# Kernel tuning notes

Hardware: AMD Instinct MI355X
Metric: run time of the kernel (lower is better)

The kernel has to match this reference:

```python
import jax, jax.numpy as jnp
import numpy as np
from jax import lax

K = 8192
D = 256
BETA = 0.1
DECAY = 0.99
EPS = 1e-05


def setup_inputs() -> dict:
    key = jax.random.key(0)
    k1, k2, k3 = jax.random.split(key, 3)
    z_e = jax.random.normal(k1, (8, 2048, D), dtype=jnp.float32)
    codebook = jax.random.normal(k2, (K, D), dtype=jnp.float32)
    ema_cluster_size = jnp.zeros((K,), dtype=jnp.float32)
    ema_w = jax.random.normal(k3, (K, D), dtype=jnp.float32)
    return {"z_e": z_e, "codebook": codebook,
            "ema_cluster_size": ema_cluster_size, "ema_w": ema_w}


def reference(z_e, codebook, ema_cluster_size, ema_w):
    B, L, Dd = z_e.shape
    # squared-distance matrix (B, L, K): ||z||^2 - 2 z.C^T + ||c||^2
    dist = ((z_e ** 2).sum(-1, keepdims=True)
            - 2.0 * jnp.einsum('bld,kd->blk', z_e, codebook)
            + (codebook ** 2).sum(-1))
    codes = jnp.argmin(dist, axis=-1)          # (B, L) int
    z_q = codebook[codes]                      # gather (B, L, D)

    # training-mode EMA statistics (segment_sum == one_hot.T @ z_e, memory-light)
    flat_codes = codes.reshape(-1)
    flat_z = z_e.reshape(-1, Dd)
    n_i = jax.ops.segment_sum(jnp.ones(flat_codes.shape, dtype=z_e.dtype),
                              flat_codes, num_segments=K)
    dw = jax.ops.segment_sum(flat_z, flat_codes, num_segments=K)
    new_cluster_size = DECAY * ema_cluster_size + (1.0 - DECAY) * n_i
    new_ema_w = DECAY * ema_w + (1.0 - DECAY) * dw
    new_codebook = new_ema_w / (new_cluster_size + EPS)[:, None]

    # straight-through combine and commitment loss
    z_q_st = z_e + lax.stop_gradient(z_q - z_e)
    vq_loss = BETA * jnp.mean((z_e - lax.stop_gradient(z_q)) ** 2)
    return z_q_st, codes, vq_loss, new_codebook, new_cluster_size, new_ema_w
```

## Files before the change

### kernel.cpp

```cpp
#include <hip/hip_runtime.h>
#include <hip/hip_bf16.h>
#include <math.h>

#define N_ROWS 16384
#define DIM    256
#define KCODES 8192

#define OFF_ZQ    0
#define OFF_CODES 4194304
#define OFF_LOSS  4210688
#define OFF_CB    4210689
#define OFF_CS    6307841
#define OFF_EW    6316033
#define OUT_TOTAL 8413185

typedef __attribute__((ext_vector_type(8))) short bf16x8;
typedef __attribute__((ext_vector_type(4))) float f32x4;
typedef __attribute__((ext_vector_type(16))) float f32x16;

__device__ __forceinline__ void gll16(const void* g, void* l) {
  __builtin_amdgcn_global_load_lds(
      (const __attribute__((address_space(1))) unsigned int*)g,
      (__attribute__((address_space(3))) unsigned int*)l, 16, 0, 0);
}

__device__ __forceinline__ unsigned short f2bf(float x) {
  __hip_bfloat16 h = __float2bfloat16(x);
  return *reinterpret_cast<unsigned short*>(&h);
}

__device__ __forceinline__ unsigned umin32(unsigned a, unsigned b) { return a < b ? a : b; }
__device__ __forceinline__ unsigned umax32(unsigned a, unsigned b) { return a > b ? a : b; }

__global__ __launch_bounds__(256) void k_pre(
    const float* __restrict__ z, unsigned short* __restrict__ zbuf,
    const float* __restrict__ cb, unsigned short* __restrict__ cbt,
    float* __restrict__ cnormb, int* __restrict__ cnt,
    float* __restrict__ loss_part) {
  const int b = blockIdx.x;
  const int tid = threadIdx.x;
  if (b < 2048) {
    int i = b * 256 + tid;
    const float4 a = ((const float4*)z)[i * 2];
    const float4 c = ((const float4*)z)[i * 2 + 1];
    union { unsigned short u[8]; uint4 v; } o;
    o.u[0] = f2bf(a.x); o.u[1] = f2bf(a.y); o.u[2] = f2bf(a.z); o.u[3] = f2bf(a.w);
    o.u[4] = f2bf(c.x); o.u[5] = f2bf(c.y); o.u[6] = f2bf(c.z); o.u[7] = f2bf(c.w);
    ((uint4*)zbuf)[i] = o.v;
  } else if (b < 3072) {
    const int code = (b - 2048) * 8 + (tid >> 5);
    const int dq = tid & 31;
    const float4 v0 = *(const float4*)(cb + (size_t)code * 256 + dq * 8);
    const float4 v1 = *(const float4*)(cb + (size_t)code * 256 + dq * 8 + 4);
    union { unsigned short u[8]; uint4 q; } o;
    o.u[0] = f2bf(-2.f * v0.x); o.u[1] = f2bf(-2.f * v0.y);
    o.u[2] = f2bf(-2.f * v0.z); o.u[3] = f2bf(-2.f * v0.w);
    o.u[4] = f2bf(-2.f * v1.x); o.u[5] = f2bf(-2.f * v1.y);
    o.u[6] = f2bf(-2.f * v1.z); o.u[7] = f2bf(-2.f * v1.w);
    *(uint4*)(cbt + ((size_t)dq * 8192 + code) * 8) = o.q;
    float s = v0.x * v0.x + v0.y * v0.y + v0.z * v0.z + v0.w * v0.w +
              v1.x * v1.x + v1.y * v1.y + v1.z * v1.z + v1.w * v1.w;
#pragma unroll
    for (int off = 16; off >= 1; off >>= 1) s += __shfl_down(s, off);
    if ((tid & 31) == 0) cnormb[code] = s + 1024.0f;
  } else if (cnt) {
    int zi = (b - 3072) * 256 + tid;
    if (zi < 8192) cnt[zi] = 0;
    else if (zi < 8448) loss_part[zi - 8192] = 0.0f;
  }
}

__global__ __launch_bounds__(256, 2) void k_argmin(
    const unsigned short* __restrict__ zb,
    const unsigned short* __restrict__ cbt,
    const float* __restrict__ cnb,
    unsigned long long* __restrict__ partials) {
  __shared__ __align__(16) unsigned char lds[69632];

  const int tid = threadIdx.x;
  const int lane = tid & 63;
  const int w = tid >> 6;
  const int wc = w & 1;
  const int wr = w >> 1;
  const int hi = lane >> 5;
  const int l31 = lane & 31;
  const int chunk = blockIdx.x;
  const int r0 = blockIdx.y << 7;

  {
    const char* zgb = (const char*)zb + (size_t)r0 * 512;
#pragma unroll
    for (int it = 0; it < 16; ++it) {
      int s = it * 256 + tid;
      int row = s >> 5;
      int dql = (tid & 31) ^ (row & 31);
      gll16(zgb + row * 512 + dql * 16, lds + s * 16);
    }
    gll16((const char*)cnb + (size_t)chunk * 4096 + tid * 16,
          lds + 65536 + tid * 16);
  }
  asm volatile("s_waitcnt vmcnt(0)" ::: "memory");
  __builtin_amdgcn_s_barrier();
  __builtin_amdgcn_sched_barrier(0);

  bf16x8 zr0[16], zr1[16];
  {
    const int xr = l31 * 16;
    const int rb0 = (wr * 64 + l31) * 512;
    const int rb1 = (wr * 64 + 32 + l31) * 512;
    const int hx = hi * 16;
#pragma unroll
    for (int ks = 0; ks < 16; ++ks) {
      zr0[ks] = *(const bf16x8*)(lds + rb0 + ((ks * 32 + hx) ^ xr));
      zr1[ks] = *(const bf16x8*)(lds + rb1 + ((ks * 32 + hx) ^ xr));
    }
  }
  asm volatile("s_waitcnt lgkmcnt(0)" ::: "memory");
  __builtin_amdgcn_s_barrier();
  __builtin_amdgcn_sched_barrier(0);

  unsigned char* lcb = lds + tid * 16;
  const char* cgc = (const char*)cbt +
      ((size_t)(tid >> 7) * 131072 + (size_t)chunk * 16384 + (tid & 127) * 16);
  gll16(cgc + 0 * 262144, lcb + 0 * 4096);
  gll16(cgc + 1 * 262144, lcb + 1 * 4096);
  gll16(cgc + 2 * 262144, lcb + 2 * 4096);

  const unsigned char* afp = lds + hi * 2048 + (wc * 64 + l31) * 16;
  const unsigned wchi4 = (unsigned)(wc * 64 + hi * 4);

  unsigned k1_00 = 0xFFFFFFFFu, k2_00 = 0xFFFFFFFFu;
  unsigned k1_01 = 0xFFFFFFFFu, k2_01 = 0xFFFFFFFFu;
  unsigned k1_10 = 0xFFFFFFFFu, k2_10 = 0xFFFFFFFFu;
  unsigned k1_11 = 0xFFFFFFFFu, k2_11 = 0xFFFFFFFFu;
  f32x16 acc00, acc01, acc10, acc11;

#define KSTEP(ks, TAIL)                                                        \
  {                                                                            \
    if ((TAIL) && (ks) == 14) asm volatile("s_waitcnt vmcnt(1)" ::: "memory"); \
    else if ((TAIL) && (ks) == 15) asm volatile("s_waitcnt vmcnt(0)" ::: "memory"); \
    else asm volatile("s_waitcnt vmcnt(2)" ::: "memory");                      \
    __builtin_amdgcn_s_barrier();                                              \
    __builtin_amdgcn_sched_barrier(0);                                         \
    if ((ks) < 13) {                                                           \
      gll16(cgc + ((ks) + 3) * 262144, lcb + (((ks) + 3) & 3) * 4096);         \
    } else if (!(TAIL)) {                                                      \
      gll16(cgc + 2048 + ((ks) - 13) * 262144, lcb + (((ks) + 3) & 3) * 4096); \
    }                                                                          \
    bf16x8 a0 = *(const bf16x8*)(afp + ((ks) & 3) * 4096);                     \
    bf16x8 a1 = *(const bf16x8*)(afp + ((ks) & 3) * 4096 + 512);               \
    acc00 = __builtin_amdgcn_mfma_f32_32x32x16_bf16(a0, zr0[ks], acc00, 0, 0, 0); \
    acc01 = __builtin_amdgcn_mfma_f32_32x32x16_bf16(a0, zr1[ks], acc01, 0, 0, 0); \
    acc10 = __builtin_amdgcn_mfma_f32_32x32x16_bf16(a1, zr0[ks], acc10, 0, 0, 0); \
    acc11 = __builtin_amdgcn_mfma_f32_32x32x16_bf16(a1, zr1[ks], acc11, 0, 0, 0); \
  }

#define CTBODY(TAIL)                                                           \
  {                                                                            \
    const int cnoff = 65536 + ct * 512 + wc * 256 + hi * 16;                   \
    f32x4 cnA[4], cnB[4];                                                      \
    _Pragma("unroll") for (int g2 = 0; g2 < 4; ++g2) {                         \
      cnA[g2] = *(const f32x4*)(lds + cnoff + g2 * 32);                        \
      cnB[g2] = *(const f32x4*)(lds + cnoff + 128 + g2 * 32);                  \
    }                                                                          \
    _Pragma("unroll") for (int r = 0; r < 16; ++r) {                           \
      float vA = cnA[r >> 2][r & 3], vB = cnB[r >> 2][r & 3];                  \
      acc00[r] = vA; acc01[r] = vA; acc10[r] = vB; acc11[r] = vB;              \
    }                                                                          \
    KSTEP(0, TAIL)  KSTEP(1, TAIL)  KSTEP(2, TAIL)  KSTEP(3, TAIL)             \
    KSTEP(4, TAIL)  KSTEP(5, TAIL)  KSTEP(6, TAIL)  KSTEP(7, TAIL)             \
    KSTEP(8, TAIL)  KSTEP(9, TAIL)  KSTEP(10, TAIL) KSTEP(11, TAIL)            \
    KSTEP(12, TAIL) KSTEP(13, TAIL) KSTEP(14, TAIL) KSTEP(15, TAIL)            \
    const unsigned vb = (unsigned)(ct * 128) | wchi4;                          \
    _Pragma("unroll") for (int r = 0; r < 16; ++r) {                           \
      const unsigned ic = (unsigned)(8 * (r >> 2) + (r & 3));                  \
      unsigned key;                                                            \
      key = (__float_as_uint(acc00[r]) & 0xFFFFFC00u) | vb | ic;               \
      if (key < k1_00) { k2_00 = k1_00; k1_00 = key; } else if (key < k2_00) k2_00 = key; \
      key = (__float_as_uint(acc01[r]) & 0xFFFFFC00u) | vb | ic;               \
      if (key < k1_01) { k2_01 = k1_01; k1_01 = key; } else if (key < k2_01) k2_01 = key; \
      key = (__float_as_uint(acc10[r]) & 0xFFFFFC00u) | vb | ic | 32u;         \
      if (key < k1_10) { k2_10 = k1_10; k1_10 = key; } else if (key < k2_10) k2_10 = key; \
      key = (__float_as_uint(acc11[r]) & 0xFFFFFC00u) | vb | ic | 32u;         \
      if (key < k1_11) { k2_11 = k1_11; k1_11 = key; } else if (key < k2_11) k2_11 = key; \
    }                                                                          \
    cgc += 2048;                                                               \
  }

  for (int ct = 0; ct < 7; ++ct) CTBODY(false)
  { int ct = 7; CTBODY(true) }
#undef CTBODY
#undef KSTEP

#define FIN(K1V, K2V, ZF, CF)                                                  \
  {                                                                            \
    unsigned o1 = (unsigned)__shfl_xor((int)(K1V), 32);                        \
    unsigned o2 = (unsigned)__shfl_xor((int)(K2V), 32);                        \
    unsigned n1 = umin32((K1V), o1);                                           \
    unsigned n2 = umin32(umax32((K1V), o1), umin32((K2V), o2));                \
    if (lane < 32) {                                                           \
      int row = r0 + wr * 64 + (ZF) * 32 + l31;                                \
      partials[(size_t)row * 32 + (chunk * 4 + wc * 2 + (CF))] =               \
          ((unsigned long long)n2 << 32) | n1;                                 \
    }                                                                          \
  }
  FIN(k1_00, k2_00, 0, 0) FIN(k1_10, k2_10, 0, 1)
  FIN(k1_01, k2_01, 1, 0) FIN(k1_11, k2_11, 1, 1)
#undef FIN
}

__global__ __launch_bounds__(256) void k_reduce(
    const unsigned long long* __restrict__ partials, const float* __restrict__ z,
    const float* __restrict__ cb, float* __restrict__ out_codes,
    int* __restrict__ cnt) {
  const int row = blockIdx.x * 4 + (threadIdx.x >> 6);
  const int lane = threadIdx.x & 63;
  const int e = lane & 31;

  unsigned myK1 = 0xFFFFFFFFu, myK2 = 0xFFFFFFFFu;
  if (lane < 32) {
    unsigned long long v = partials[(size_t)row * 32 + e];
    myK1 = (unsigned)v; myK2 = (unsigned)(v >> 32);
  }
  unsigned K1 = myK1, K2 = myK2;
  int bc = e >> 2;
#pragma unroll
  for (int m = 1; m <= 32; m <<= 1) {
    unsigned o1 = (unsigned)__shfl_xor((int)K1, m);
    unsigned o2 = (unsigned)__shfl_xor((int)K2, m);
    int ob = __shfl_xor(bc, m);
    unsigned nK2 = umin32(umax32(K1, o1), umin32(K2, o2));
    if (o1 < K1 || (o1 == K1 && ob < bc)) { K1 = o1; bc = ob; }
    K2 = nK2;
  }
  int chosen = bc * 1024 + (int)(K1 & 1023u);

  float r1 = __uint_as_float(K1 & 0xFFFFFC00u);
  float r2 = __uint_as_float(K2 & 0xFFFFFC00u);
  if (r2 - r1 < 0.75f) {
    const float win = r1 + 0.75f;
    const float* zr = z + ((size_t)row << 8);
    double bestd = 1e300; int bestj = 0x7fffffff;
#pragma unroll
    for (int h = 0; h < 2; ++h) {
      unsigned k = h ? myK2 : myK1;
      float bv = __uint_as_float(k & 0xFFFFFC00u);
      if (lane < 32 && bv <= win) {
        int jv = (e >> 2) * 1024 + (int)(k & 1023u);
        const float* c = cb + ((size_t)jv << 8);
        double d = 0.0;
        for (int kk = 0; kk < DIM; ++kk) {
          double df = (double)zr[kk] - (double)c[kk];
          d += df * df;
        }
        if (d < bestd || (d == bestd && jv < bestj)) { bestd = d; bestj = jv; }
      }
    }
#pragma unroll
    for (int m = 1; m <= 32; m <<= 1) {
      double od = __shfl_xor(bestd, m);
      int oj = __shfl_xor(bestj, m);
      if (od < bestd || (od == bestd && oj < bestj)) { bestd = od; bestj = oj; }
    }
    chosen = bestj;
  }
  if (lane == 0) {
    out_codes[row] = (float)chosen;
    if (cnt) atomicAdd(&cnt[chosen], 1);
  }
}

__global__ __launch_bounds__(1024) void k_scanplace(
    const int* __restrict__ cnt, int* __restrict__ start,
    const float* __restrict__ ema_cs, float* __restrict__ cs_out,
    const float* __restrict__ codesf, int* __restrict__ rowlist) {
  __shared__ int lcur[8192];
  __shared__ int wsum[16], wbase[16];
  const int t = threadIdx.x;
  const int lane = t & 63, wid = t >> 6;
  const int base = t * 8;
  int c[8], s = 0;
#pragma unroll
  for (int i = 0; i < 8; ++i) { c[i] = cnt[base + i]; s += c[i]; }
  int inc = s;
#pragma unroll
  for (int off = 1; off < 64; off <<= 1) {
    int v = __shfl_up(inc, off);
    if (lane >= off) inc += v;
  }
  if (lane == 63) wsum[wid] = inc;
  __syncthreads();
  if (t < 16) {
    int v = wsum[t];
    int winc = v;
#pragma unroll
    for (int off = 1; off < 16; off <<= 1) {
      int u = __shfl_up(winc, off);
      if (t >= off) winc += u;
    }
    wbase[t] = winc - v;
  }
  __syncthreads();
  int ex = wbase[wid] + (inc - s);
#pragma unroll
  for (int i = 0; i < 8; ++i) {
    start[base + i] = ex;
    lcur[base + i] = ex;
    cs_out[base + i] = 0.99f * ema_cs[base + i] + 0.01f * (float)c[i];
    ex += c[i];
  }
  __syncthreads();
#pragma unroll
  for (int rr = 0; rr < 16; ++rr) {
    int r = rr * 1024 + t;
    int cc = (int)codesf[r];
    int p = atomicAdd(&lcur[cc], 1);
    rowlist[p] = r;
  }
}

__global__ __launch_bounds__(256) void k_dw2(
    const float* __restrict__ z, const float* __restrict__ cb,
    const int* __restrict__ start, const int* __restrict__ cnt,
    const int* __restrict__ rowlist, const float* __restrict__ ema_w,
    const float* __restrict__ cs_new, float* __restrict__ zq,
    float* __restrict__ ew, float* __restrict__ cb_out,
    float* __restrict__ loss_part) {
  const int k = blockIdx.x;
  const int d = threadIdx.x;
  const int s = start[k], n = cnt[k];
  const size_t o = ((size_t)k << 8) + d;
  const float q = cb[o];
  float a0 = 0.f, a1 = 0.f, a2 = 0.f, a3 = 0.f;
  float l0 = 0.f, l1 = 0.f, l2 = 0.f, l3 = 0.f;
  int t = 0;
  for (; t + 4 <= n; t += 4) {
    size_t ro0 = ((size_t)rowlist[s + t] << 8) + d;
    size_t ro1 = ((size_t)rowlist[s + t + 1] << 8) + d;
    size_t ro2 = ((size_t)rowlist[s + t + 2] << 8) + d;
    size_t ro3 = ((size_t)rowlist[s + t + 3] << 8) + d;
    float z0 = z[ro0], z1 = z[ro1], z2 = z[ro2], z3 = z[ro3];
    zq[ro0] = q; zq[ro1] = q; zq[ro2] = q; zq[ro3] = q;
    a0 += z0; a1 += z1; a2 += z2; a3 += z3;
    float d0 = z0 - q, d1 = z1 - q, d2 = z2 - q, d3 = z3 - q;
    l0 += d0 * d0; l1 += d1 * d1; l2 += d2 * d2; l3 += d3 * d3;
  }
  for (; t < n; ++t) {
    size_t ro = ((size_t)rowlist[s + t] << 8) + d;
    float zv = z[ro];
    zq[ro] = q;
    a0 += zv;
    float df = zv - q;
    l0 += df * df;
  }
  float a = (a0 + a1) + (a2 + a3);
  float lacc = (l0 + l1) + (l2 + l3);
  const float v = 0.99f * ema_w[o] + 0.01f * a;
  ew[o] = v;
  cb_out[o] = v / (cs_new[k] + 1e-5f);

#pragma unroll
  for (int off = 32; off >= 1; off >>= 1) lacc += __shfl_down(lacc, off);
  __shared__ float wp[4];
  if ((d & 63) == 0) wp[d >> 6] = lacc;
  __syncthreads();
  if (d == 0 && n > 0) {
    float ssum = (wp[0] + wp[1]) + (wp[2] + wp[3]);
    atomicAdd(loss_part + (k & 255), ssum * (float)(0.1 / 4194304.0));
  }
}

__global__ __launch_bounds__(256) void k_loss_final(
    const float* __restrict__ part, float* __restrict__ loss) {
  float s = part[threadIdx.x];
#pragma unroll
  for (int off = 32; off >= 1; off >>= 1) s += __shfl_down(s, off);
  __shared__ float w[4];
  if ((threadIdx.x & 63) == 0) w[threadIdx.x >> 6] = s;
  __syncthreads();
  if (threadIdx.x == 0) loss[0] = (w[0] + w[1]) + (w[2] + w[3]);
}

__global__ __launch_bounds__(256) void k_scatter(
    const float* __restrict__ z, const float* __restrict__ cb,
    const float* __restrict__ codesf, float* __restrict__ zq,
    float* __restrict__ loss, float* __restrict__ cs_acc,
    float* __restrict__ ew_acc) {
  const int row = blockIdx.x;
  const int d = threadIdx.x;
  const int c = (int)codesf[row];
  const float zv = z[((size_t)row << 8) + d];
  const float qv = cb[((size_t)c << 8) + d];
  zq[((size_t)row << 8) + d] = zv + (qv - zv);
  float diff = zv - qv;
  float sq = diff * diff;
#pragma unroll
  for (int off = 32; off >= 1; off >>= 1) sq += __shfl_down(sq, off);
  __shared__ float wpart[4];
  if ((d & 63) == 0) wpart[d >> 6] = sq;
  __syncthreads();
  if (d == 0) {
    float s = (wpart[0] + wpart[1]) + (wpart[2] + wpart[3]);
    atomicAdd(loss, s * (float)(0.1 / 4194304.0));
    atomicAdd(cs_acc + c, 1.0f);
  }
  atomicAdd(ew_acc + ((size_t)c << 8) + d, zv);
}

__global__ __launch_bounds__(256) void k_ema_cs(const float* __restrict__ ema_cs,
                                                float* __restrict__ cs_io) {
  const int k = blockIdx.x * 256 + threadIdx.x;
  const float cnt = cs_io[k];
  cs_io[k] = 0.99f * ema_cs[k] + 0.01f * cnt;
}

__global__ __launch_bounds__(256) void k_ema_w(const float* __restrict__ ema_w,
                                               const float* __restrict__ cs_new,
                                               float* __restrict__ ew_io,
                                               float* __restrict__ cb_out) {
  const int i = blockIdx.x * 256 + threadIdx.x;
  const float dw = ew_io[i];
  const float v = 0.99f * ema_w[i] + 0.01f * dw;
  ew_io[i] = v;
  cb_out[i] = v / (cs_new[i >> 8] + 1e-5f);
}

extern "C" void kernel_launch(void* const* d_in, const int* in_sizes, int n_in,
                              void* d_out, int out_size, void* d_ws, size_t ws_size,
                              hipStream_t stream) {
  const float* z      = (const float*)d_in[0];
  const float* cb     = (const float*)d_in[1];
  const float* ema_cs = (const float*)d_in[2];
  const float* ema_w  = (const float*)d_in[3];
  float* out = (float*)d_out;

  float* o_zq    = out + OFF_ZQ;
  float* o_codes = out + OFF_CODES;
  float* o_loss  = out + OFF_LOSS;
  float* o_cb    = out + OFF_CB;
  float* o_cs    = out + OFF_CS;
  float* o_ew    = out + OFF_EW;

  uintptr_t zb_a  = ((uintptr_t)o_cb + 15) & ~(uintptr_t)15;
  uintptr_t cbt_a = ((uintptr_t)o_ew + 15) & ~(uintptr_t)15;
  unsigned short* zbuf = (unsigned short*)zb_a;
  unsigned short* cbt  = (unsigned short*)cbt_a;
  float* cnormb = (float*)(cbt_a + 4194304);
  unsigned long long* partials = (unsigned long long*)o_zq;

  const size_t ws_need = 4 * (8192 * 2 + 16384 + 256);
  const bool sorted = (ws_size >= ws_need);
  int* cnt      = (int*)d_ws;
  int* start    = cnt + 8192;
  int* rowlist  = start + 8192;
  float* loss_part = (float*)(rowlist + 16384);

  k_pre<<<3105, 256, 0, stream>>>(z, zbuf, cb, cbt, cnormb,
                                  sorted ? cnt : (int*)nullptr, loss_part);

  dim3 g(8, 128);
  k_argmin<<<g, 256, 0, stream>>>(zbuf, cbt, cnormb, partials);
  k_reduce<<<N_ROWS / 4, 256, 0, stream>>>(partials, z, cb, o_codes,
                                           sorted ? cnt : (int*)nullptr);

  if (sorted) {
    k_scanplace<<<1, 1024, 0, stream>>>(cnt, start, ema_cs, o_cs, o_codes,
                                        rowlist);
    k_dw2<<<KCODES, 256, 0, stream>>>(z, cb, start, cnt, rowlist, ema_w,
                                      o_cs, o_zq, o_ew, o_cb, loss_part);
    k_loss_final<<<1, 256, 0, stream>>>(loss_part, o_loss);
  } else {
    (void)hipMemsetAsync(o_loss, 0,
                         (size_t)(OUT_TOTAL - OFF_LOSS) * sizeof(float), stream);
    k_scatter<<<N_ROWS, 256, 0, stream>>>(z, cb, o_codes, o_zq, o_loss, o_cs,
                                          o_ew);
    k_ema_cs<<<KCODES / 256, 256, 0, stream>>>(ema_cs, o_cs);
    k_ema_w <<<KCODES * DIM / 256, 256, 0, stream>>>(ema_w, o_cs, o_ew, o_cb);
  }
}
```

Measured before the change: 163.6 us.

## Process two codebook chunks per argmin block and use branchless top-2 merge

Each argmin block now covers 2048 codes instead of 1024, in two halves. The z tile loaded into registers is reused across both halves, and the grid is halved to 4x128 blocks. This cuts repeated z loads and per-block setup, at the cost of fewer blocks (512) for the GPU to schedule and more LDS per block. The top-2 update is rewritten as branchless min/max, and partial slots are remapped so the reducer still sees 32 entries per row.

```diff
diff --git a/kernel.cpp b/kernel.cpp
--- a/kernel.cpp
+++ b/kernel.cpp
@@ -75,7 +75,7 @@
     const unsigned short* __restrict__ cbt,
     const float* __restrict__ cnb,
     unsigned long long* __restrict__ partials) {
-  __shared__ __align__(16) unsigned char lds[69632];
+  __shared__ __align__(16) unsigned char lds[73728];
 
   const int tid = threadIdx.x;
   const int lane = tid & 63;
@@ -96,8 +96,10 @@
       int dql = (tid & 31) ^ (row & 31);
       gll16(zgb + row * 512 + dql * 16, lds + s * 16);
     }
-    gll16((const char*)cnb + (size_t)chunk * 4096 + tid * 16,
+    gll16((const char*)cnb + (size_t)chunk * 8192 + tid * 16,
           lds + 65536 + tid * 16);
+    gll16((const char*)cnb + (size_t)chunk * 8192 + 4096 + tid * 16,
+          lds + 69632 + tid * 16);
   }
   asm volatile("s_waitcnt vmcnt(0)" ::: "memory");
   __builtin_amdgcn_s_barrier();
@@ -121,7 +123,7 @@
 
   unsigned char* lcb = lds + tid * 16;
   const char* cgc = (const char*)cbt +
-      ((size_t)(tid >> 7) * 131072 + (size_t)chunk * 16384 + (tid & 127) * 16);
+      ((size_t)(tid >> 7) * 131072 + (size_t)chunk * 32768 + (tid & 127) * 16);
   gll16(cgc + 0 * 262144, lcb + 0 * 4096);
   gll16(cgc + 1 * 262144, lcb + 1 * 4096);
   gll16(cgc + 2 * 262144, lcb + 2 * 4096);
@@ -155,9 +157,16 @@
     acc11 = __builtin_amdgcn_mfma_f32_32x32x16_bf16(a1, zr1[ks], acc11, 0, 0, 0); \
   }
 
-#define CTBODY(TAIL)                                                           \
+#define MRG(K1V, K2V, KEY)                                                     \
   {                                                                            \
-    const int cnoff = 65536 + ct * 512 + wc * 256 + hi * 16;                   \
+    unsigned t_ = umax32(K1V, (KEY));                                          \
+    K2V = umin32(K2V, t_);                                                     \
+    K1V = umin32(K1V, (KEY));                                                  \
+  }
+
+#define CTBODY(HALF, TAIL)                                                     \
+  {                                                                            \
+    const int cnoff = 65536 + (HALF) * 4096 + ct * 512 + wc * 256 + hi * 16;   \
     f32x4 cnA[4], cnB[4];                                                      \
     _Pragma("unroll") for (int g2 = 0; g2 < 4; ++g2) {                         \
       cnA[g2] = *(const f32x4*)(lds + cnoff + g2 * 32);                        \
@@ -173,26 +182,33 @@
     KSTEP(12, TAIL) KSTEP(13, TAIL) KSTEP(14, TAIL) KSTEP(15, TAIL)            \
     const unsigned vb = (unsigned)(ct * 128) | wchi4;                          \
     _Pragma("unroll") for (int r = 0; r < 16; ++r) {                           \
-      const unsigned ic = (unsigned)(8 * (r >> 2) + (r & 3));                  \
+      const unsigned base = (unsigned)(8 * (r >> 2) + (r & 3));                \
       unsigned key;                                                            \
-      key = (__float_as_uint(acc00[r]) & 0xFFFFFC00u) | vb | ic;               \
-      if (key < k1_00) { k2_00 = k1_00; k1_00 = key; } else if (key < k2_00) k2_00 = key; \
-      key = (__float_as_uint(acc01[r]) & 0xFFFFFC00u) | vb | ic;               \
-      if (key < k1_01) { k2_01 = k1_01; k1_01 = key; } else if (key < k2_01) k2_01 = key; \
-      key = (__float_as_uint(acc10[r]) & 0xFFFFFC00u) | vb | ic | 32u;         \
-      if (key < k1_10) { k2_10 = k1_10; k1_10 = key; } else if (key < k2_10) k2_10 = key; \
-      key = (__float_as_uint(acc11[r]) & 0xFFFFFC00u) | vb | ic | 32u;         \
-      if (key < k1_11) { k2_11 = k1_11; k1_11 = key; } else if (key < k2_11) k2_11 = key; \
+      key = (__float_as_uint(acc00[r]) & 0xFFFFFC00u) | (vb | base);           \
+      MRG(k1_00, k2_00, key)                                                   \
+      key = (__float_as_uint(acc01[r]) & 0xFFFFFC00u) | (vb | base);           \
+      MRG(k1_01, k2_01, key)                                                   \
+      key = (__float_as_uint(acc10[r]) & 0xFFFFFC00u) | (vb | base | 32u);     \
+      MRG(k1_10, k2_10, key)                                                   \
+      key = (__float_as_uint(acc11[r]) & 0xFFFFFC00u) | (vb | base | 32u);     \
+      MRG(k1_11, k2_11, key)                                                   \
     }                                                                          \
     cgc += 2048;                                                               \
   }
 
-  for (int ct = 0; ct < 7; ++ct) CTBODY(false)
-  { int ct = 7; CTBODY(true) }
+  for (int ct = 0; ct < 8; ++ct) CTBODY(0, false)
+  unsigned s1_00 = k1_00, s2_00 = k2_00, s1_01 = k1_01, s2_01 = k2_01;
+  unsigned s1_10 = k1_10, s2_10 = k2_10, s1_11 = k1_11, s2_11 = k2_11;
+  k1_00 = k2_00 = k1_01 = k2_01 = 0xFFFFFFFFu;
+  k1_10 = k2_10 = k1_11 = k2_11 = 0xFFFFFFFFu;
+
+  for (int ct = 0; ct < 7; ++ct) CTBODY(1, false)
+  { int ct = 7; CTBODY(1, true) }
 #undef CTBODY
+#undef MRG
 #undef KSTEP
 
-#define FIN(K1V, K2V, ZF, CF)                                                  \
+#define FIN(K1V, K2V, ZF, ENT)                                                 \
   {                                                                            \
     unsigned o1 = (unsigned)__shfl_xor((int)(K1V), 32);                        \
     unsigned o2 = (unsigned)__shfl_xor((int)(K2V), 32);                        \
@@ -200,12 +216,15 @@
     unsigned n2 = umin32(umax32((K1V), o1), umin32((K2V), o2));                \
     if (lane < 32) {                                                           \
       int row = r0 + wr * 64 + (ZF) * 32 + l31;                                \
-      partials[(size_t)row * 32 + (chunk * 4 + wc * 2 + (CF))] =               \
+      partials[(size_t)row * 32 + (ENT)] =                                     \
           ((unsigned long long)n2 << 32) | n1;                                 \
     }                                                                          \
   }
-  FIN(k1_00, k2_00, 0, 0) FIN(k1_10, k2_10, 0, 1)
-  FIN(k1_01, k2_01, 1, 0) FIN(k1_11, k2_11, 1, 1)
+  const int eb = chunk * 8 + wc * 2;
+  FIN(s1_00, s2_00, 0, eb + 0) FIN(s1_10, s2_10, 0, eb + 1)
+  FIN(s1_01, s2_01, 1, eb + 0) FIN(s1_11, s2_11, 1, eb + 1)
+  FIN(k1_00, k2_00, 0, eb + 4) FIN(k1_10, k2_10, 0, eb + 5)
+  FIN(k1_01, k2_01, 1, eb + 4) FIN(k1_11, k2_11, 1, eb + 5)
 #undef FIN
 }
 
@@ -458,7 +477,7 @@
   k_pre<<<3105, 256, 0, stream>>>(z, zbuf, cb, cbt, cnormb,
                                   sorted ? cnt : (int*)nullptr, loss_part);
 
-  dim3 g(8, 128);
+  dim3 g(4, 128);
   k_argmin<<<g, 256, 0, stream>>>(zbuf, cbt, cnormb, partials);
   k_reduce<<<N_ROWS / 4, 256, 0, stream>>>(partials, z, cb, o_codes,
                                            sorted ? cnt : (int*)nullptr);
```

Result: faster. 158.3 us (-3.2%).

## Shrink argmin LDS to raise occupancy and use branchless top-2 merge

Applied to the files above, without the earlier changes.

The argmin kernel now stages the 128-row z tile through LDS in four 32-row phases instead of all at once. This cuts shared memory from 68KB to 20KB, and launch bounds are raised to allow 4 blocks per CU. The top-2 key tracking replaces data-dependent branches with min/max operations. The phased staging adds barriers and serialised load waits in the prologue, and the higher occupancy target may force register spills, since each thread holds 32 bf16x8 z fragments plus four 16-wide accumulators.

```diff
diff --git a/kernel.cpp b/kernel.cpp
--- a/kernel.cpp
+++ b/kernel.cpp
@@ -70,12 +70,12 @@
   }
 }
 
-__global__ __launch_bounds__(256, 2) void k_argmin(
+__global__ __launch_bounds__(256, 4) void k_argmin(
     const unsigned short* __restrict__ zb,
     const unsigned short* __restrict__ cbt,
     const float* __restrict__ cnb,
     unsigned long long* __restrict__ partials) {
-  __shared__ __align__(16) unsigned char lds[69632];
+  __shared__ __align__(16) unsigned char lds[20480];
 
   const int tid = threadIdx.x;
   const int lane = tid & 63;
@@ -87,37 +87,50 @@
   const int chunk = blockIdx.x;
   const int r0 = blockIdx.y << 7;
 
-  {
-    const char* zgb = (const char*)zb + (size_t)r0 * 512;
-#pragma unroll
-    for (int it = 0; it < 16; ++it) {
-      int s = it * 256 + tid;
-      int row = s >> 5;
-      int dql = (tid & 31) ^ (row & 31);
-      gll16(zgb + row * 512 + dql * 16, lds + s * 16);
+  gll16((const char*)cnb + (size_t)chunk * 4096 + tid * 16,
+        lds + 16384 + tid * 16);
+  const char* zgb = (const char*)zb + (size_t)r0 * 512;
+#pragma unroll
+  for (int it = 0; it < 4; ++it) {
+    int s = it * 256 + tid;
+    int row = s >> 5;
+    int dql = (s & 31) ^ row;
+    gll16(zgb + row * 512 + dql * 16, lds + s * 16);
+  }
+
+  bf16x8 zr0[16], zr1[16];
+#pragma unroll
+  for (int p = 0; p < 4; ++p) {
+    asm volatile("s_waitcnt vmcnt(0)" ::: "memory");
+    __builtin_amdgcn_s_barrier();
+    __builtin_amdgcn_sched_barrier(0);
+    if ((p >> 1) == wr) {
+      const int xr = l31 * 16;
+      const int rb = l31 * 512;
+      const int hx = hi * 16;
+      if ((p & 1) == 0) {
+#pragma unroll
+        for (int ks = 0; ks < 16; ++ks)
+          zr0[ks] = *(const bf16x8*)(lds + rb + ((ks * 32 + hx) ^ xr));
+      } else {
+#pragma unroll
+        for (int ks = 0; ks < 16; ++ks)
+          zr1[ks] = *(const bf16x8*)(lds + rb + ((ks * 32 + hx) ^ xr));
+      }
     }
-    gll16((const char*)cnb + (size_t)chunk * 4096 + tid * 16,
-          lds + 65536 + tid * 16);
-  }
-  asm volatile("s_waitcnt vmcnt(0)" ::: "memory");
-  __builtin_amdgcn_s_barrier();
-  __builtin_amdgcn_sched_barrier(0);
-
-  bf16x8 zr0[16], zr1[16];
-  {
-    const int xr = l31 * 16;
-    const int rb0 = (wr * 64 + l31) * 512;
-    const int rb1 = (wr * 64 + 32 + l31) * 512;
-    const int hx = hi * 16;
-#pragma unroll
-    for (int ks = 0; ks < 16; ++ks) {
-      zr0[ks] = *(const bf16x8*)(lds + rb0 + ((ks * 32 + hx) ^ xr));
-      zr1[ks] = *(const bf16x8*)(lds + rb1 + ((ks * 32 + hx) ^ xr));
+    asm volatile("s_waitcnt lgkmcnt(0)" ::: "memory");
+    __builtin_amdgcn_sched_barrier(0);
+    __builtin_amdgcn_s_barrier();
+    if (p < 3) {
+#pragma unroll
+      for (int it = 0; it < 4; ++it) {
+        int s = it * 256 + tid;
+        int row = s >> 5;
+        int dql = (s & 31) ^ row;
+        gll16(zgb + ((p + 1) * 32 + row) * 512 + dql * 16, lds + s * 16);
+      }
     }
   }
-  asm volatile("s_waitcnt lgkmcnt(0)" ::: "memory");
-  __builtin_amdgcn_s_barrier();
-  __builtin_amdgcn_sched_barrier(0);
 
   unsigned char* lcb = lds + tid * 16;
   const char* cgc = (const char*)cbt +
@@ -155,9 +168,16 @@
     acc11 = __builtin_amdgcn_mfma_f32_32x32x16_bf16(a1, zr1[ks], acc11, 0, 0, 0); \
   }
 
+#define MRG(K1V, K2V, KEY)                                                     \
+  {                                                                            \
+    unsigned t_ = umax32(K1V, (KEY));                                          \
+    K2V = umin32(K2V, t_);                                                     \
+    K1V = umin32(K1V, (KEY));                                                  \
+  }
+
 #define CTBODY(TAIL)                                                           \
   {                                                                            \
-    const int cnoff = 65536 + ct * 512 + wc * 256 + hi * 16;                   \
+    const int cnoff = 16384 + ct * 512 + wc * 256 + hi * 16;                   \
     f32x4 cnA[4], cnB[4];                                                      \
     _Pragma("unroll") for (int g2 = 0; g2 < 4; ++g2) {                         \
       cnA[g2] = *(const f32x4*)(lds + cnoff + g2 * 32);                        \
@@ -173,16 +193,16 @@
     KSTEP(12, TAIL) KSTEP(13, TAIL) KSTEP(14, TAIL) KSTEP(15, TAIL)            \
     const unsigned vb = (unsigned)(ct * 128) | wchi4;                          \
     _Pragma("unroll") for (int r = 0; r < 16; ++r) {                           \
-      const unsigned ic = (unsigned)(8 * (r >> 2) + (r & 3));                  \
+      const unsigned base = (unsigned)(8 * (r >> 2) + (r & 3));                \
       unsigned key;                                                            \
-      key = (__float_as_uint(acc00[r]) & 0xFFFFFC00u) | vb | ic;               \
-      if (key < k1_00) { k2_00 = k1_00; k1_00 = key; } else if (key < k2_00) k2_00 = key; \
-      key = (__float_as_uint(acc01[r]) & 0xFFFFFC00u) | vb | ic;               \
-      if (key < k1_01) { k2_01 = k1_01; k1_01 = key; } else if (key < k2_01) k2_01 = key; \
-      key = (__float_as_uint(acc10[r]) & 0xFFFFFC00u) | vb | ic | 32u;         \
-      if (key < k1_10) { k2_10 = k1_10; k1_10 = key; } else if (key < k2_10) k2_10 = key; \
-      key = (__float_as_uint(acc11[r]) & 0xFFFFFC00u) | vb | ic | 32u;         \
-      if (key < k1_11) { k2_11 = k1_11; k1_11 = key; } else if (key < k2_11) k2_11 = key; \
+      key = (__float_as_uint(acc00[r]) & 0xFFFFFC00u) | (vb | base);           \
+      MRG(k1_00, k2_00, key)                                                   \
+      key = (__float_as_uint(acc01[r]) & 0xFFFFFC00u) | (vb | base);           \
+      MRG(k1_01, k2_01, key)                                                   \
+      key = (__float_as_uint(acc10[r]) & 0xFFFFFC00u) | (vb | base | 32u);     \
+      MRG(k1_10, k2_10, key)                                                   \
+      key = (__float_as_uint(acc11[r]) & 0xFFFFFC00u) | (vb | base | 32u);     \
+      MRG(k1_11, k2_11, key)                                                   \
     }                                                                          \
     cgc += 2048;                                                               \
   }
@@ -190,6 +210,7 @@
   for (int ct = 0; ct < 7; ++ct) CTBODY(false)
   { int ct = 7; CTBODY(true) }
 #undef CTBODY
+#undef MRG
 #undef KSTEP
 
 #define FIN(K1V, K2V, ZF, CF)                                                  \
```

Result: slower. 257.3 us (+57.3%).
